# Optimization experiments

Hardware: AMD Instinct MI355X
Metric: run time of the kernel (lower is better)

## Reference

```python
import math
import jax, jax.numpy as jnp
import numpy as np

S, B, H = 512, 64, 1024

def setup_inputs() -> dict:
    key = jax.random.key(0)
    ks = jax.random.split(key, 7)
    hidden = jax.random.normal(ks[0], (1, B, H), dtype=jnp.float32)
    encoder_outputs = jax.random.normal(ks[1], (S, B, H), dtype=jnp.float32)
    pe = jax.random.normal(ks[2], (B, S), dtype=jnp.float32)
    seq_mask = jax.random.bernoulli(ks[3], 0.1, (B, S))
    # nn.Linear(2H, H): weight (H, 2H), bias (H); nn.Linear(H, 1, bias=False): weight (1, H)
    Wa = jax.random.normal(ks[4], (H, 2 * H), dtype=jnp.float32) * (1.0 / math.sqrt(2 * H))
    ba = jax.random.normal(ks[5], (H,), dtype=jnp.float32) * 0.01
    Ws = jax.random.normal(ks[6], (1, H), dtype=jnp.float32) * (1.0 / math.sqrt(H))
    return {"hidden": hidden, "encoder_outputs": encoder_outputs, "pe": pe,
            "seq_mask": seq_mask, "Wa": Wa, "ba": ba, "Ws": Ws}

def reference(hidden, encoder_outputs, pe, seq_mask, Wa, ba, Ws):
    max_len, bsz, hdim = encoder_outputs.shape
    factor = 1.0 / math.sqrt(hdim)
    scale = factor * math.log(max_len)
    # repeat hidden along seq dim, concat on feature dim -> (S, B, 2H)
    h_rep = jnp.broadcast_to(hidden, (max_len, bsz, hdim))
    energy_in = jnp.concatenate([h_rep, encoder_outputs], axis=2)  # (S, B, 2H)
    e = jax.nn.relu(jnp.einsum('sbf,hf->sbh', energy_in, Wa) + ba)  # (S, B, H)
    attn = scale * jnp.einsum('sbh,oh->sbo', e, Ws)[..., 0]          # (S, B)
    attn = attn.T + pe                                               # (B, S)
    attn = jnp.where(seq_mask, jnp.float32(-1e12), attn)
    attn = jax.nn.softmax(attn, axis=1)
    return attn[:, None, :]  # (B, 1, S)
```

## Files before the change

### kernel.cpp

```cpp
#include <hip/hip_runtime.h>
#include <hip/hip_bf16.h>

#define S_LEN 512
#define HDIM 1024
#define H2 2048

typedef float f32x4 __attribute__((ext_vector_type(4)));
typedef float f32x2 __attribute__((ext_vector_type(2)));
typedef __bf16 bf16x8 __attribute__((ext_vector_type(8)));

#define E1_PITCH 258
__global__ __launch_bounds__(256) void k_e1(const float* __restrict__ hidden,
                                            const float* __restrict__ Wa,
                                            const float* __restrict__ ba,
                                            float* __restrict__ e1) {
    __shared__ float hsh[64 * E1_PITCH];
    int h = blockIdx.x * 4 + (threadIdx.x >> 6);
    int lane = threadIdx.x & 63;
    const float* wrow = Wa + (size_t)h * H2;
    float acc = 0.f;
    for (int k0 = 0; k0 < HDIM; k0 += 256) {
        __syncthreads();
        for (int idx = threadIdx.x; idx < 4096; idx += 256) {
            int b = idx >> 6, ck = (idx & 63) << 2;
            f32x4 v = *(const f32x4*)(hidden + b * HDIM + k0 + ck);
            f32x2 lo; lo[0] = v[0]; lo[1] = v[1];
            f32x2 hi; hi[0] = v[2]; hi[1] = v[3];
            *(f32x2*)(hsh + b * E1_PITCH + ck) = lo;
            *(f32x2*)(hsh + b * E1_PITCH + ck + 2) = hi;
        }
        __syncthreads();
        const float* wr = wrow + k0;
        const float* hb = hsh + lane * E1_PITCH;
#pragma unroll 8
        for (int kk = 0; kk < 256; kk += 4) {
            f32x4 w = *(const f32x4*)(wr + kk);
            f32x2 h01 = *(const f32x2*)(hb + kk);
            f32x2 h23 = *(const f32x2*)(hb + kk + 2);
            acc += w[0] * h01[0] + w[1] * h01[1] + w[2] * h23[0] + w[3] * h23[1];
        }
    }
    e1[lane * HDIM + h] = acc + ba[h];
}

__global__ __launch_bounds__(256) void k_packB(const float* __restrict__ Wa,
                                               unsigned short* __restrict__ wsB,
                                               float* __restrict__ logits) {
    int ci = blockIdx.x * 256 + threadIdx.x;
    if (ci < S_LEN * 64) logits[ci] = 0.f;
    int tile = ci >> 9;
    int wi = ci & 511;
    int row = wi >> 2;
    int slot = wi & 3;
    int nt = tile >> 5, kt = tile & 31;
    int n = nt * 128 + row;
    int kk = kt * 32 + ((slot ^ ((row >> 1) & 3)) << 3);
    const float* src = Wa + (size_t)n * H2 + HDIM + kk;
    f32x4 a = *(const f32x4*)src;
    f32x4 b = *(const f32x4*)(src + 4);
    bf16x8 o;
    o[0] = (__bf16)a[0]; o[1] = (__bf16)a[1]; o[2] = (__bf16)a[2]; o[3] = (__bf16)a[3];
    o[4] = (__bf16)b[0]; o[5] = (__bf16)b[1]; o[6] = (__bf16)b[2]; o[7] = (__bf16)b[3];
    *(bf16x8*)(wsB + (size_t)ci * 8) = o;
}

__global__ __launch_bounds__(256) void k_main(const float* __restrict__ enc,
                                              const unsigned short* __restrict__ wsB,
                                              const float* __restrict__ e1,
                                              const float* __restrict__ Ws,
                                              float* __restrict__ logits) {
    __shared__ __align__(16) unsigned short As[4096];
    __shared__ __align__(16) unsigned short Bs[4096];

    int i = blockIdx.x;
    int mt = ((i >> 6) << 3) | (i & 7);
    int nt = (i >> 3) & 7;
    int r0 = mt * 128;
    int n0 = nt * 128;

    int tid = threadIdx.x;
    int lane = tid & 63, wid = tid >> 6;
    int wr = wid >> 1, wc = wid & 1;
    int c = lane & 15, g = lane >> 4;

    int rowA = tid >> 2;
    int slotA = tid & 3;
    int kkA = (slotA ^ ((rowA >> 1) & 3)) << 3;
    const float* aptr0 = enc + (size_t)(r0 + rowA) * HDIM + kkA;
    const float* aptr1 = aptr0 + (size_t)64 * HDIM;

    f32x4 acc[4][4] = {};

    f32x4 c0 = *(const f32x4*)(aptr0);
    f32x4 c1 = *(const f32x4*)(aptr0 + 4);
    f32x4 c2 = *(const f32x4*)(aptr1);
    f32x4 c3 = *(const f32x4*)(aptr1 + 4);

    for (int kt = 0; kt < 32; ++kt) {
        const unsigned short* bsrc = wsB + ((size_t)(nt * 32 + kt) << 12);
        char* lb = (char*)Bs + wid * 1024;
        __builtin_amdgcn_global_load_lds(
            (const __attribute__((address_space(1))) void*)(bsrc + (size_t)tid * 8),
            (__attribute__((address_space(3))) void*)lb, 16, 0, 0);
        __builtin_amdgcn_global_load_lds(
            (const __attribute__((address_space(1))) void*)(bsrc + (size_t)(tid + 256) * 8),
            (__attribute__((address_space(3))) void*)(lb + 4096), 16, 0, 0);
        __builtin_amdgcn_sched_barrier(0);

        int kn = (kt < 31) ? kt + 1 : 31;
        f32x4 n0v = *(const f32x4*)(aptr0 + kn * 32);
        f32x4 n1v = *(const f32x4*)(aptr0 + kn * 32 + 4);
        f32x4 n2v = *(const f32x4*)(aptr1 + kn * 32);
        f32x4 n3v = *(const f32x4*)(aptr1 + kn * 32 + 4);

        bf16x8 o0, o1;
        o0[0] = (__bf16)c0[0]; o0[1] = (__bf16)c0[1]; o0[2] = (__bf16)c0[2]; o0[3] = (__bf16)c0[3];
        o0[4] = (__bf16)c1[0]; o0[5] = (__bf16)c1[1]; o0[6] = (__bf16)c1[2]; o0[7] = (__bf16)c1[3];
        o1[0] = (__bf16)c2[0]; o1[1] = (__bf16)c2[1]; o1[2] = (__bf16)c2[2]; o1[3] = (__bf16)c2[3];
        o1[4] = (__bf16)c3[0]; o1[5] = (__bf16)c3[1]; o1[6] = (__bf16)c3[2]; o1[7] = (__bf16)c3[3];
        *(bf16x8*)((char*)As + (rowA << 6) + (slotA << 4)) = o0;
        *(bf16x8*)((char*)As + ((rowA + 64) << 6) + (slotA << 4)) = o1;

        asm volatile("s_waitcnt vmcnt(4) lgkmcnt(0)" ::: "memory");
        __builtin_amdgcn_sched_barrier(0);
        __builtin_amdgcn_s_barrier();
        __builtin_amdgcn_sched_barrier(0);

        bf16x8 af[4], bfr[4];
#pragma unroll
        for (int m = 0; m < 4; ++m) {
            int row = wr * 64 + m * 16 + c;
            int slot = g ^ ((row >> 1) & 3);
            af[m] = *(const bf16x8*)((const char*)As + row * 64 + slot * 16);
        }
#pragma unroll
        for (int n = 0; n < 4; ++n) {
            int rowb = wc * 64 + n * 16 + c;
            int slot = g ^ ((rowb >> 1) & 3);
            bfr[n] = *(const bf16x8*)((const char*)Bs + rowb * 64 + slot * 16);
        }
#pragma unroll
        for (int m = 0; m < 4; ++m)
#pragma unroll
            for (int n = 0; n < 4; ++n)
                acc[m][n] = __builtin_amdgcn_mfma_f32_16x16x32_bf16(af[m], bfr[n], acc[m][n], 0, 0, 0);

        __builtin_amdgcn_sched_barrier(0);
        __builtin_amdgcn_s_barrier();
        __builtin_amdgcn_sched_barrier(0);

        c0 = n0v; c1 = n1v; c2 = n2v; c3 = n3v;
    }

    float wsv[4];
#pragma unroll
    for (int n = 0; n < 4; ++n) wsv[n] = Ws[n0 + wc * 64 + n * 16 + c];

#pragma unroll
    for (int m = 0; m < 4; ++m) {
#pragma unroll
        for (int j = 0; j < 4; ++j) {
            int rl = wr * 64 + m * 16 + g * 4 + j;
            int r = r0 + rl;
            int b = r & 63, sidx = r >> 6;
            const float* e1b = e1 + b * HDIM + n0 + wc * 64;
            float p = 0.f;
#pragma unroll
            for (int n = 0; n < 4; ++n) {
                float v = acc[m][n][j] + e1b[n * 16 + c];
                v = fmaxf(v, 0.f);
                p += v * wsv[n];
            }
            p += __shfl_xor(p, 1);
            p += __shfl_xor(p, 2);
            p += __shfl_xor(p, 4);
            p += __shfl_xor(p, 8);
            if (c == 0) atomicAdd(&logits[b * S_LEN + sidx], p);
        }
    }
}

__global__ __launch_bounds__(512) void k_softmax(float* __restrict__ out,
                                                 const float* __restrict__ pe,
                                                 const int* __restrict__ mask,
                                                 float scale) {
    __shared__ float red[8];
    int b = blockIdx.x, s = threadIdx.x;
    int idx = (b << 9) + s;
    float acc = out[idx];
    float logit = (mask[idx] != 0) ? -1e12f : (scale * acc + pe[idx]);
    float m = logit;
#pragma unroll
    for (int o = 32; o >= 1; o >>= 1) m = fmaxf(m, __shfl_xor(m, o));
    if ((s & 63) == 0) red[s >> 6] = m;
    __syncthreads();
    float m2 = red[0];
#pragma unroll
    for (int i2 = 1; i2 < 8; ++i2) m2 = fmaxf(m2, red[i2]);
    float e = expf(logit - m2);
    float t = e;
#pragma unroll
    for (int o = 32; o >= 1; o >>= 1) t += __shfl_xor(t, o);
    __syncthreads();
    if ((s & 63) == 0) red[s >> 6] = t;
    __syncthreads();
    float tot = 0.f;
#pragma unroll
    for (int i2 = 0; i2 < 8; ++i2) tot += red[i2];
    out[idx] = e / tot;
}

extern "C" void kernel_launch(void* const* d_in, const int* in_sizes, int n_in,
                              void* d_out, int out_size, void* d_ws, size_t ws_size,
                              hipStream_t stream) {
    const float* hidden = (const float*)d_in[0];
    const float* enc    = (const float*)d_in[1];
    const float* pe     = (const float*)d_in[2];
    const int*   mask   = (const int*)d_in[3];
    const float* Wa     = (const float*)d_in[4];
    const float* ba     = (const float*)d_in[5];
    const float* Ws     = (const float*)d_in[6];
    float* out = (float*)d_out;

    float* e1 = (float*)d_ws;
    unsigned short* wsB = (unsigned short*)((char*)d_ws + 262144);

    const float scale = 0.19494764453248462f;

    k_e1<<<256, 256, 0, stream>>>(hidden, Wa, ba, e1);
    k_packB<<<512, 256, 0, stream>>>(Wa, wsB, out);
    k_main<<<2048, 256, 0, stream>>>(enc, wsB, e1, Ws, out);
    k_softmax<<<64, 512, 0, stream>>>(out, pe, mask, scale);
}
```

Baseline: 398.4 us.

## Double-buffer LDS tiles in main GEMM loop to drop one barrier per step

Doubles the A and B shared-memory tiles and alternates between two buffers. The next tile's global-to-LDS load and bf16 conversion are issued before the MFMAs on the current buffer, with encoder prefetch moved two steps ahead. This leaves one barrier per k-step instead of two. It also adds a min-blocks launch bound of 4, which doubles LDS use to 32KB per block and may limit registers.

```diff
diff --git a/kernel.cpp b/kernel.cpp
--- a/kernel.cpp
+++ b/kernel.cpp
@@ -64,13 +64,13 @@
     *(bf16x8*)(wsB + (size_t)ci * 8) = o;
 }
 
-__global__ __launch_bounds__(256) void k_main(const float* __restrict__ enc,
-                                              const unsigned short* __restrict__ wsB,
-                                              const float* __restrict__ e1,
-                                              const float* __restrict__ Ws,
-                                              float* __restrict__ logits) {
-    __shared__ __align__(16) unsigned short As[4096];
-    __shared__ __align__(16) unsigned short Bs[4096];
+__global__ __launch_bounds__(256, 4) void k_main(const float* __restrict__ enc,
+                                                 const unsigned short* __restrict__ wsB,
+                                                 const float* __restrict__ e1,
+                                                 const float* __restrict__ Ws,
+                                                 float* __restrict__ logits) {
+    __shared__ __align__(16) unsigned short As[8192];
+    __shared__ __align__(16) unsigned short Bs[8192];
 
     int i = blockIdx.x;
     int mt = ((i >> 6) << 3) | (i & 7);
@@ -88,16 +88,13 @@
     int kkA = (slotA ^ ((rowA >> 1) & 3)) << 3;
     const float* aptr0 = enc + (size_t)(r0 + rowA) * HDIM + kkA;
     const float* aptr1 = aptr0 + (size_t)64 * HDIM;
+    int awo0 = (rowA << 6) + (slotA << 4);
+    int awo1 = ((rowA + 64) << 6) + (slotA << 4);
 
     f32x4 acc[4][4] = {};
 
-    f32x4 c0 = *(const f32x4*)(aptr0);
-    f32x4 c1 = *(const f32x4*)(aptr0 + 4);
-    f32x4 c2 = *(const f32x4*)(aptr1);
-    f32x4 c3 = *(const f32x4*)(aptr1 + 4);
-
-    for (int kt = 0; kt < 32; ++kt) {
-        const unsigned short* bsrc = wsB + ((size_t)(nt * 32 + kt) << 12);
+    {
+        const unsigned short* bsrc = wsB + ((size_t)(nt * 32) << 12);
         char* lb = (char*)Bs + wid * 1024;
         __builtin_amdgcn_global_load_lds(
             (const __attribute__((address_space(1))) void*)(bsrc + (size_t)tid * 8),
@@ -105,39 +102,74 @@
         __builtin_amdgcn_global_load_lds(
             (const __attribute__((address_space(1))) void*)(bsrc + (size_t)(tid + 256) * 8),
             (__attribute__((address_space(3))) void*)(lb + 4096), 16, 0, 0);
-        __builtin_amdgcn_sched_barrier(0);
-
-        int kn = (kt < 31) ? kt + 1 : 31;
-        f32x4 n0v = *(const f32x4*)(aptr0 + kn * 32);
-        f32x4 n1v = *(const f32x4*)(aptr0 + kn * 32 + 4);
-        f32x4 n2v = *(const f32x4*)(aptr1 + kn * 32);
-        f32x4 n3v = *(const f32x4*)(aptr1 + kn * 32 + 4);
-
+    }
+    __builtin_amdgcn_sched_barrier(0);
+    f32x4 t0 = *(const f32x4*)(aptr0);
+    f32x4 t1 = *(const f32x4*)(aptr0 + 4);
+    f32x4 t2 = *(const f32x4*)(aptr1);
+    f32x4 t3 = *(const f32x4*)(aptr1 + 4);
+    f32x4 p0 = *(const f32x4*)(aptr0 + 32);
+    f32x4 p1 = *(const f32x4*)(aptr0 + 36);
+    f32x4 p2 = *(const f32x4*)(aptr1 + 32);
+    f32x4 p3 = *(const f32x4*)(aptr1 + 36);
+    {
         bf16x8 o0, o1;
-        o0[0] = (__bf16)c0[0]; o0[1] = (__bf16)c0[1]; o0[2] = (__bf16)c0[2]; o0[3] = (__bf16)c0[3];
-        o0[4] = (__bf16)c1[0]; o0[5] = (__bf16)c1[1]; o0[6] = (__bf16)c1[2]; o0[7] = (__bf16)c1[3];
-        o1[0] = (__bf16)c2[0]; o1[1] = (__bf16)c2[1]; o1[2] = (__bf16)c2[2]; o1[3] = (__bf16)c2[3];
-        o1[4] = (__bf16)c3[0]; o1[5] = (__bf16)c3[1]; o1[6] = (__bf16)c3[2]; o1[7] = (__bf16)c3[3];
-        *(bf16x8*)((char*)As + (rowA << 6) + (slotA << 4)) = o0;
-        *(bf16x8*)((char*)As + ((rowA + 64) << 6) + (slotA << 4)) = o1;
-
-        asm volatile("s_waitcnt vmcnt(4) lgkmcnt(0)" ::: "memory");
-        __builtin_amdgcn_sched_barrier(0);
-        __builtin_amdgcn_s_barrier();
-        __builtin_amdgcn_sched_barrier(0);
+        o0[0] = (__bf16)t0[0]; o0[1] = (__bf16)t0[1]; o0[2] = (__bf16)t0[2]; o0[3] = (__bf16)t0[3];
+        o0[4] = (__bf16)t1[0]; o0[5] = (__bf16)t1[1]; o0[6] = (__bf16)t1[2]; o0[7] = (__bf16)t1[3];
+        o1[0] = (__bf16)t2[0]; o1[1] = (__bf16)t2[1]; o1[2] = (__bf16)t2[2]; o1[3] = (__bf16)t2[3];
+        o1[4] = (__bf16)t3[0]; o1[5] = (__bf16)t3[1]; o1[6] = (__bf16)t3[2]; o1[7] = (__bf16)t3[3];
+        *(bf16x8*)((char*)As + awo0) = o0;
+        *(bf16x8*)((char*)As + awo1) = o1;
+    }
+    asm volatile("s_waitcnt vmcnt(4) lgkmcnt(0)" ::: "memory");
+    __builtin_amdgcn_sched_barrier(0);
+    __builtin_amdgcn_s_barrier();
+    __builtin_amdgcn_sched_barrier(0);
+
+#pragma unroll 2
+    for (int t = 0; t < 32; ++t) {
+        int cb = (t & 1) << 13;
+        int nb = cb ^ 8192;
+
+        if (t < 31) {
+            const unsigned short* bsrc = wsB + ((size_t)(nt * 32 + t + 1) << 12);
+            char* lbw = (char*)Bs + nb + wid * 1024;
+            __builtin_amdgcn_global_load_lds(
+                (const __attribute__((address_space(1))) void*)(bsrc + (size_t)tid * 8),
+                (__attribute__((address_space(3))) void*)lbw, 16, 0, 0);
+            __builtin_amdgcn_global_load_lds(
+                (const __attribute__((address_space(1))) void*)(bsrc + (size_t)(tid + 256) * 8),
+                (__attribute__((address_space(3))) void*)(lbw + 4096), 16, 0, 0);
+            __builtin_amdgcn_sched_barrier(0);
+
+            int kn = (t + 2 < 32) ? t + 2 : 31;
+            f32x4 q0 = *(const f32x4*)(aptr0 + kn * 32);
+            f32x4 q1 = *(const f32x4*)(aptr0 + kn * 32 + 4);
+            f32x4 q2 = *(const f32x4*)(aptr1 + kn * 32);
+            f32x4 q3 = *(const f32x4*)(aptr1 + kn * 32 + 4);
+
+            bf16x8 o0, o1;
+            o0[0] = (__bf16)p0[0]; o0[1] = (__bf16)p0[1]; o0[2] = (__bf16)p0[2]; o0[3] = (__bf16)p0[3];
+            o0[4] = (__bf16)p1[0]; o0[5] = (__bf16)p1[1]; o0[6] = (__bf16)p1[2]; o0[7] = (__bf16)p1[3];
+            o1[0] = (__bf16)p2[0]; o1[1] = (__bf16)p2[1]; o1[2] = (__bf16)p2[2]; o1[3] = (__bf16)p2[3];
+            o1[4] = (__bf16)p3[0]; o1[5] = (__bf16)p3[1]; o1[6] = (__bf16)p3[2]; o1[7] = (__bf16)p3[3];
+            *(bf16x8*)((char*)As + nb + awo0) = o0;
+            *(bf16x8*)((char*)As + nb + awo1) = o1;
+            p0 = q0; p1 = q1; p2 = q2; p3 = q3;
+        }
 
         bf16x8 af[4], bfr[4];
 #pragma unroll
         for (int m = 0; m < 4; ++m) {
             int row = wr * 64 + m * 16 + c;
             int slot = g ^ ((row >> 1) & 3);
-            af[m] = *(const bf16x8*)((const char*)As + row * 64 + slot * 16);
+            af[m] = *(const bf16x8*)((const char*)As + cb + row * 64 + slot * 16);
         }
 #pragma unroll
         for (int n = 0; n < 4; ++n) {
             int rowb = wc * 64 + n * 16 + c;
             int slot = g ^ ((rowb >> 1) & 3);
-            bfr[n] = *(const bf16x8*)((const char*)Bs + rowb * 64 + slot * 16);
+            bfr[n] = *(const bf16x8*)((const char*)Bs + cb + rowb * 64 + slot * 16);
         }
 #pragma unroll
         for (int m = 0; m < 4; ++m)
@@ -145,11 +177,12 @@
             for (int n = 0; n < 4; ++n)
                 acc[m][n] = __builtin_amdgcn_mfma_f32_16x16x32_bf16(af[m], bfr[n], acc[m][n], 0, 0, 0);
 
-        __builtin_amdgcn_sched_barrier(0);
-        __builtin_amdgcn_s_barrier();
-        __builtin_amdgcn_sched_barrier(0);
-
-        c0 = n0v; c1 = n1v; c2 = n2v; c3 = n3v;
+        if (t < 31) {
+            asm volatile("s_waitcnt vmcnt(4) lgkmcnt(0)" ::: "memory");
+            __builtin_amdgcn_sched_barrier(0);
+            __builtin_amdgcn_s_barrier();
+            __builtin_amdgcn_sched_barrier(0);
+        }
     }
 
     float wsv[4];
```

Result: faster. 371.7 us (-6.7%).

## Double K-tile depth to 64 per stage with 8-slot XOR swizzle

Applied to the files above, without the earlier changes.

The main GEMM kernel now processes K in 16 steps of 64 instead of 32 steps of 32. This halves the number of barrier pairs and load/convert phases, and the LDS tiles and B pre-packing are re-laid out with a row^slot XOR swizzle over 8 slots. It also raises MFMA wave priority around the compute block. In exchange it doubles LDS use per block and the register use for prefetched A (16 f32x4), which may lower occupancy.

```diff
diff --git a/kernel.cpp b/kernel.cpp
--- a/kernel.cpp
+++ b/kernel.cpp
@@ -48,13 +48,13 @@
                                                float* __restrict__ logits) {
     int ci = blockIdx.x * 256 + threadIdx.x;
     if (ci < S_LEN * 64) logits[ci] = 0.f;
-    int tile = ci >> 9;
-    int wi = ci & 511;
-    int row = wi >> 2;
-    int slot = wi & 3;
-    int nt = tile >> 5, kt = tile & 31;
+    int tile = ci >> 10;
+    int wi = ci & 1023;
+    int row = wi >> 3;
+    int slot = wi & 7;
+    int nt = tile >> 4, kt = tile & 15;
     int n = nt * 128 + row;
-    int kk = kt * 32 + ((slot ^ ((row >> 1) & 3)) << 3);
+    int kk = kt * 64 + ((slot ^ (row & 7)) << 3);
     const float* src = Wa + (size_t)n * H2 + HDIM + kk;
     f32x4 a = *(const f32x4*)src;
     f32x4 b = *(const f32x4*)(src + 4);
@@ -69,8 +69,8 @@
                                               const float* __restrict__ e1,
                                               const float* __restrict__ Ws,
                                               float* __restrict__ logits) {
-    __shared__ __align__(16) unsigned short As[4096];
-    __shared__ __align__(16) unsigned short Bs[4096];
+    __shared__ __align__(16) unsigned short As[8192];
+    __shared__ __align__(16) unsigned short Bs[8192];
 
     int i = blockIdx.x;
     int mt = ((i >> 6) << 3) | (i & 7);
@@ -83,73 +83,89 @@
     int wr = wid >> 1, wc = wid & 1;
     int c = lane & 15, g = lane >> 4;
 
-    int rowA = tid >> 2;
-    int slotA = tid & 3;
-    int kkA = (slotA ^ ((rowA >> 1) & 3)) << 3;
-    const float* aptr0 = enc + (size_t)(r0 + rowA) * HDIM + kkA;
-    const float* aptr1 = aptr0 + (size_t)64 * HDIM;
+    int row0 = tid >> 3;
+    int slotA = tid & 7;
+    int colBase = ((slotA ^ (row0 & 7)) << 3);
+    const float* abase = enc + (size_t)(r0 + row0) * HDIM + colBase;
 
     f32x4 acc[4][4] = {};
-
-    f32x4 c0 = *(const f32x4*)(aptr0);
-    f32x4 c1 = *(const f32x4*)(aptr0 + 4);
-    f32x4 c2 = *(const f32x4*)(aptr1);
-    f32x4 c3 = *(const f32x4*)(aptr1 + 4);
-
-    for (int kt = 0; kt < 32; ++kt) {
-        const unsigned short* bsrc = wsB + ((size_t)(nt * 32 + kt) << 12);
-        char* lb = (char*)Bs + wid * 1024;
-        __builtin_amdgcn_global_load_lds(
-            (const __attribute__((address_space(1))) void*)(bsrc + (size_t)tid * 8),
-            (__attribute__((address_space(3))) void*)lb, 16, 0, 0);
-        __builtin_amdgcn_global_load_lds(
-            (const __attribute__((address_space(1))) void*)(bsrc + (size_t)(tid + 256) * 8),
-            (__attribute__((address_space(3))) void*)(lb + 4096), 16, 0, 0);
-        __builtin_amdgcn_sched_barrier(0);
-
-        int kn = (kt < 31) ? kt + 1 : 31;
-        f32x4 n0v = *(const f32x4*)(aptr0 + kn * 32);
-        f32x4 n1v = *(const f32x4*)(aptr0 + kn * 32 + 4);
-        f32x4 n2v = *(const f32x4*)(aptr1 + kn * 32);
-        f32x4 n3v = *(const f32x4*)(aptr1 + kn * 32 + 4);
-
-        bf16x8 o0, o1;
-        o0[0] = (__bf16)c0[0]; o0[1] = (__bf16)c0[1]; o0[2] = (__bf16)c0[2]; o0[3] = (__bf16)c0[3];
-        o0[4] = (__bf16)c1[0]; o0[5] = (__bf16)c1[1]; o0[6] = (__bf16)c1[2]; o0[7] = (__bf16)c1[3];
-        o1[0] = (__bf16)c2[0]; o1[1] = (__bf16)c2[1]; o1[2] = (__bf16)c2[2]; o1[3] = (__bf16)c2[3];
-        o1[4] = (__bf16)c3[0]; o1[5] = (__bf16)c3[1]; o1[6] = (__bf16)c3[2]; o1[7] = (__bf16)c3[3];
-        *(bf16x8*)((char*)As + (rowA << 6) + (slotA << 4)) = o0;
-        *(bf16x8*)((char*)As + ((rowA + 64) << 6) + (slotA << 4)) = o1;
-
-        asm volatile("s_waitcnt vmcnt(4) lgkmcnt(0)" ::: "memory");
+    f32x4 p[8], q[8];
+
+#pragma unroll
+    for (int it = 0; it < 4; ++it) {
+        const float* ap = abase + (size_t)it * 32 * HDIM;
+        p[2 * it]     = *(const f32x4*)(ap);
+        p[2 * it + 1] = *(const f32x4*)(ap + 4);
+    }
+
+#pragma unroll 2
+    for (int t = 0; t < 16; ++t) {
+        const unsigned short* bsrc = wsB + ((size_t)(nt * 16 + t) << 13);
+#pragma unroll
+        for (int it = 0; it < 4; ++it) {
+            __builtin_amdgcn_global_load_lds(
+                (const __attribute__((address_space(1))) void*)(bsrc + (size_t)(tid + it * 256) * 8),
+                (__attribute__((address_space(3))) void*)((char*)Bs + it * 4096 + wid * 1024),
+                16, 0, 0);
+        }
+        __builtin_amdgcn_sched_barrier(0);
+
+        {
+            int tn = (t < 15) ? t + 1 : 15;
+            const float* an = abase + tn * 64;
+#pragma unroll
+            for (int it = 0; it < 4; ++it) {
+                const float* ap = an + (size_t)it * 32 * HDIM;
+                q[2 * it]     = *(const f32x4*)(ap);
+                q[2 * it + 1] = *(const f32x4*)(ap + 4);
+            }
+        }
+        __builtin_amdgcn_sched_barrier(0);
+
+#pragma unroll
+        for (int it = 0; it < 4; ++it) {
+            bf16x8 o;
+            f32x4 lo = p[2 * it], hi = p[2 * it + 1];
+            o[0] = (__bf16)lo[0]; o[1] = (__bf16)lo[1]; o[2] = (__bf16)lo[2]; o[3] = (__bf16)lo[3];
+            o[4] = (__bf16)hi[0]; o[5] = (__bf16)hi[1]; o[6] = (__bf16)hi[2]; o[7] = (__bf16)hi[3];
+            *(bf16x8*)((char*)As + (size_t)(tid + it * 256) * 16) = o;
+        }
+
+        asm volatile("s_waitcnt vmcnt(8) lgkmcnt(0)" ::: "memory");
         __builtin_amdgcn_sched_barrier(0);
         __builtin_amdgcn_s_barrier();
         __builtin_amdgcn_sched_barrier(0);
 
-        bf16x8 af[4], bfr[4];
-#pragma unroll
-        for (int m = 0; m < 4; ++m) {
-            int row = wr * 64 + m * 16 + c;
-            int slot = g ^ ((row >> 1) & 3);
-            af[m] = *(const bf16x8*)((const char*)As + row * 64 + slot * 16);
-        }
-#pragma unroll
-        for (int n = 0; n < 4; ++n) {
-            int rowb = wc * 64 + n * 16 + c;
-            int slot = g ^ ((rowb >> 1) & 3);
-            bfr[n] = *(const bf16x8*)((const char*)Bs + rowb * 64 + slot * 16);
-        }
-#pragma unroll
-        for (int m = 0; m < 4; ++m)
-#pragma unroll
-            for (int n = 0; n < 4; ++n)
-                acc[m][n] = __builtin_amdgcn_mfma_f32_16x16x32_bf16(af[m], bfr[n], acc[m][n], 0, 0, 0);
+#pragma unroll
+        for (int ks = 0; ks < 2; ++ks) {
+            bf16x8 af[4], bfr[4];
+#pragma unroll
+            for (int m = 0; m < 4; ++m) {
+                int row = wr * 64 + m * 16 + c;
+                int sl = (ks * 4 + g) ^ (row & 7);
+                af[m] = *(const bf16x8*)((const char*)As + row * 128 + sl * 16);
+            }
+#pragma unroll
+            for (int n = 0; n < 4; ++n) {
+                int rowb = wc * 64 + n * 16 + c;
+                int sl = (ks * 4 + g) ^ (rowb & 7);
+                bfr[n] = *(const bf16x8*)((const char*)Bs + rowb * 128 + sl * 16);
+            }
+            __builtin_amdgcn_s_setprio(1);
+#pragma unroll
+            for (int m = 0; m < 4; ++m)
+#pragma unroll
+                for (int n = 0; n < 4; ++n)
+                    acc[m][n] = __builtin_amdgcn_mfma_f32_16x16x32_bf16(af[m], bfr[n], acc[m][n], 0, 0, 0);
+            __builtin_amdgcn_s_setprio(0);
+        }
 
         __builtin_amdgcn_sched_barrier(0);
         __builtin_amdgcn_s_barrier();
         __builtin_amdgcn_sched_barrier(0);
 
-        c0 = n0v; c1 = n1v; c2 = n2v; c3 = n3v;
+#pragma unroll
+        for (int r = 0; r < 8; ++r) p[r] = q[r];
     }
 
     float wsv[4];
@@ -164,18 +180,18 @@
             int r = r0 + rl;
             int b = r & 63, sidx = r >> 6;
             const float* e1b = e1 + b * HDIM + n0 + wc * 64;
-            float p = 0.f;
+            float pp = 0.f;
 #pragma unroll
             for (int n = 0; n < 4; ++n) {
                 float v = acc[m][n][j] + e1b[n * 16 + c];
                 v = fmaxf(v, 0.f);
-                p += v * wsv[n];
-            }
-            p += __shfl_xor(p, 1);
-            p += __shfl_xor(p, 2);
-            p += __shfl_xor(p, 4);
-            p += __shfl_xor(p, 8);
-            if (c == 0) atomicAdd(&logits[b * S_LEN + sidx], p);
+                pp += v * wsv[n];
+            }
+            pp += __shfl_xor(pp, 1);
+            pp += __shfl_xor(pp, 2);
+            pp += __shfl_xor(pp, 4);
+            pp += __shfl_xor(pp, 8);
+            if (c == 0) atomicAdd(&logits[b * S_LEN + sidx], pp);
         }
     }
 }
```

Result: faster. 383.4 us (-3.8%).

## Double-buffer A and B tiles via direct global-to-LDS loads in main GEMM

Applied to the files above, without the earlier changes.

Encoder fp32 tiles now go straight into LDS with global_load_lds, swizzled and double-buffered alongside the pre-converted bf16 weight tiles. The fp32-to-bf16 conversion moves to the fragment read path. The next k-tile is prefetched during current compute, which removes the register staging and the wait between store and barrier. It also raises MFMA wave priority and sets a three-blocks-per-CU occupancy hint. In exchange, LDS use grows to 48KB and the per-iteration conversion work is repeated in every wave rather than done once per element.

```diff
diff --git a/kernel.cpp b/kernel.cpp
--- a/kernel.cpp
+++ b/kernel.cpp
@@ -64,13 +64,12 @@
     *(bf16x8*)(wsB + (size_t)ci * 8) = o;
 }
 
-__global__ __launch_bounds__(256) void k_main(const float* __restrict__ enc,
-                                              const unsigned short* __restrict__ wsB,
-                                              const float* __restrict__ e1,
-                                              const float* __restrict__ Ws,
-                                              float* __restrict__ logits) {
-    __shared__ __align__(16) unsigned short As[4096];
-    __shared__ __align__(16) unsigned short Bs[4096];
+__global__ __launch_bounds__(256, 3) void k_main(const float* __restrict__ enc,
+                                                 const unsigned short* __restrict__ wsB,
+                                                 const float* __restrict__ e1,
+                                                 const float* __restrict__ Ws,
+                                                 float* __restrict__ logits) {
+    __shared__ __align__(16) char lds[49152];
 
     int i = blockIdx.x;
     int mt = ((i >> 6) << 3) | (i & 7);
@@ -83,45 +82,48 @@
     int wr = wid >> 1, wc = wid & 1;
     int c = lane & 15, g = lane >> 4;
 
-    int rowA = tid >> 2;
-    int slotA = tid & 3;
-    int kkA = (slotA ^ ((rowA >> 1) & 3)) << 3;
-    const float* aptr0 = enc + (size_t)(r0 + rowA) * HDIM + kkA;
-    const float* aptr1 = aptr0 + (size_t)64 * HDIM;
+    int arow = tid >> 3;
+    int aslot = tid & 7;
+    int acol = (aslot ^ (arow & 7)) << 2;
+    const float* asrc0 = enc + (size_t)(r0 + arow) * HDIM + acol;
+
+    const unsigned short* bbase = wsB + ((size_t)(nt * 32) << 12);
 
     f32x4 acc[4][4] = {};
 
-    f32x4 c0 = *(const f32x4*)(aptr0);
-    f32x4 c1 = *(const f32x4*)(aptr0 + 4);
-    f32x4 c2 = *(const f32x4*)(aptr1);
-    f32x4 c3 = *(const f32x4*)(aptr1 + 4);
-
-    for (int kt = 0; kt < 32; ++kt) {
-        const unsigned short* bsrc = wsB + ((size_t)(nt * 32 + kt) << 12);
-        char* lb = (char*)Bs + wid * 1024;
-        __builtin_amdgcn_global_load_lds(
-            (const __attribute__((address_space(1))) void*)(bsrc + (size_t)tid * 8),
-            (__attribute__((address_space(3))) void*)lb, 16, 0, 0);
-        __builtin_amdgcn_global_load_lds(
-            (const __attribute__((address_space(1))) void*)(bsrc + (size_t)(tid + 256) * 8),
-            (__attribute__((address_space(3))) void*)(lb + 4096), 16, 0, 0);
-        __builtin_amdgcn_sched_barrier(0);
-
-        int kn = (kt < 31) ? kt + 1 : 31;
-        f32x4 n0v = *(const f32x4*)(aptr0 + kn * 32);
-        f32x4 n1v = *(const f32x4*)(aptr0 + kn * 32 + 4);
-        f32x4 n2v = *(const f32x4*)(aptr1 + kn * 32);
-        f32x4 n3v = *(const f32x4*)(aptr1 + kn * 32 + 4);
-
-        bf16x8 o0, o1;
-        o0[0] = (__bf16)c0[0]; o0[1] = (__bf16)c0[1]; o0[2] = (__bf16)c0[2]; o0[3] = (__bf16)c0[3];
-        o0[4] = (__bf16)c1[0]; o0[5] = (__bf16)c1[1]; o0[6] = (__bf16)c1[2]; o0[7] = (__bf16)c1[3];
-        o1[0] = (__bf16)c2[0]; o1[1] = (__bf16)c2[1]; o1[2] = (__bf16)c2[2]; o1[3] = (__bf16)c2[3];
-        o1[4] = (__bf16)c3[0]; o1[5] = (__bf16)c3[1]; o1[6] = (__bf16)c3[2]; o1[7] = (__bf16)c3[3];
-        *(bf16x8*)((char*)As + (rowA << 6) + (slotA << 4)) = o0;
-        *(bf16x8*)((char*)As + ((rowA + 64) << 6) + (slotA << 4)) = o1;
-
-        asm volatile("s_waitcnt vmcnt(4) lgkmcnt(0)" ::: "memory");
+#define STAGE_AB(AOFF, BOFF, KT)                                                        \
+    {                                                                                   \
+        const float* as_ = asrc0 + (KT) * 32;                                           \
+        _Pragma("unroll")                                                               \
+        for (int it = 0; it < 4; ++it) {                                                \
+            __builtin_amdgcn_global_load_lds(                                           \
+                (const __attribute__((address_space(1))) void*)(as_ + (size_t)it * 32 * HDIM), \
+                (__attribute__((address_space(3))) void*)(lds + (AOFF) + it * 4096 + wid * 1024), \
+                16, 0, 0);                                                              \
+        }                                                                               \
+        const unsigned short* bs_ = bbase + ((size_t)(KT) << 12);                       \
+        _Pragma("unroll")                                                               \
+        for (int it = 0; it < 2; ++it) {                                                \
+            __builtin_amdgcn_global_load_lds(                                           \
+                (const __attribute__((address_space(1))) void*)(bs_ + (size_t)(tid + it * 256) * 8), \
+                (__attribute__((address_space(3))) void*)(lds + (BOFF) + it * 4096 + wid * 1024), \
+                16, 0, 0);                                                              \
+        }                                                                               \
+    }
+
+    STAGE_AB(0, 32768, 0);
+
+#pragma unroll 2
+    for (int t = 0; t < 32; ++t) {
+        int ca = (t & 1) ? 16384 : 0;
+        int na = ca ^ 16384;
+        int cbb = (t & 1) ? 40960 : 32768;
+        int nb = cbb ^ 8192;
+        int tn = (t < 31) ? t + 1 : 31;
+
+        STAGE_AB(na, nb, tn);
+        __builtin_amdgcn_sched_barrier(0);
+        asm volatile("s_waitcnt vmcnt(6)" ::: "memory");
         __builtin_amdgcn_sched_barrier(0);
         __builtin_amdgcn_s_barrier();
         __builtin_amdgcn_sched_barrier(0);
@@ -129,28 +131,35 @@
         bf16x8 af[4], bfr[4];
 #pragma unroll
         for (int m = 0; m < 4; ++m) {
-            int row = wr * 64 + m * 16 + c;
-            int slot = g ^ ((row >> 1) & 3);
-            af[m] = *(const bf16x8*)((const char*)As + row * 64 + slot * 16);
+            int rowa = wr * 64 + m * 16 + c;
+            const char* pa = lds + ca + rowa * 128;
+            int s0 = (2 * g) ^ (rowa & 7);
+            f32x4 fa = *(const f32x4*)(pa + s0 * 16);
+            f32x4 fb = *(const f32x4*)(pa + (s0 ^ 1) * 16);
+            bf16x8 o;
+            o[0] = (__bf16)fa[0]; o[1] = (__bf16)fa[1]; o[2] = (__bf16)fa[2]; o[3] = (__bf16)fa[3];
+            o[4] = (__bf16)fb[0]; o[5] = (__bf16)fb[1]; o[6] = (__bf16)fb[2]; o[7] = (__bf16)fb[3];
+            af[m] = o;
         }
 #pragma unroll
         for (int n = 0; n < 4; ++n) {
             int rowb = wc * 64 + n * 16 + c;
-            int slot = g ^ ((rowb >> 1) & 3);
-            bfr[n] = *(const bf16x8*)((const char*)Bs + rowb * 64 + slot * 16);
-        }
+            int sl = g ^ ((rowb >> 1) & 3);
+            bfr[n] = *(const bf16x8*)(lds + cbb + rowb * 64 + sl * 16);
+        }
+        __builtin_amdgcn_s_setprio(1);
 #pragma unroll
         for (int m = 0; m < 4; ++m)
 #pragma unroll
             for (int n = 0; n < 4; ++n)
                 acc[m][n] = __builtin_amdgcn_mfma_f32_16x16x32_bf16(af[m], bfr[n], acc[m][n], 0, 0, 0);
+        __builtin_amdgcn_s_setprio(0);
 
         __builtin_amdgcn_sched_barrier(0);
         __builtin_amdgcn_s_barrier();
         __builtin_amdgcn_sched_barrier(0);
-
-        c0 = n0v; c1 = n1v; c2 = n2v; c3 = n3v;
-    }
+    }
+    asm volatile("s_waitcnt vmcnt(0)" ::: "memory");
 
     float wsv[4];
 #pragma unroll
@@ -164,20 +173,21 @@
             int r = r0 + rl;
             int b = r & 63, sidx = r >> 6;
             const float* e1b = e1 + b * HDIM + n0 + wc * 64;
-            float p = 0.f;
+            float pp = 0.f;
 #pragma unroll
             for (int n = 0; n < 4; ++n) {
                 float v = acc[m][n][j] + e1b[n * 16 + c];
                 v = fmaxf(v, 0.f);
-                p += v * wsv[n];
+                pp += v * wsv[n];
             }
-            p += __shfl_xor(p, 1);
-            p += __shfl_xor(p, 2);
-            p += __shfl_xor(p, 4);
-            p += __shfl_xor(p, 8);
-            if (c == 0) atomicAdd(&logits[b * S_LEN + sidx], p);
-        }
-    }
+            pp += __shfl_xor(pp, 1);
+            pp += __shfl_xor(pp, 2);
+            pp += __shfl_xor(pp, 4);
+            pp += __shfl_xor(pp, 8);
+            if (c == 0) atomicAdd(&logits[b * S_LEN + sidx], pp);
+        }
+    }
+#undef STAGE_AB
 }
 
 __global__ __launch_bounds__(512) void k_softmax(float* __restrict__ out,
```

Measured after the change: 355.7 us. 10.7% less time.
